# Kernel tuning notes

Measured on AMD Instinct MI355X. Metric: run time of the kernel, lower is better.

The kernel has to match this reference:

```python
import jax, jax.numpy as jnp
import numpy as np

# powers used in the generalized loss (self.range_p); static int constants
RANGE_P = (1, 2)


def setup_inputs() -> dict:
    key = jax.random.key(0)
    k1, k2, k3 = jax.random.split(key, 3)
    n, L, P = 8192, 96, len(RANGE_P)
    y_true = jax.random.normal(k1, (n, L), dtype=jnp.float32)
    y_pred = jax.random.normal(k2, (n, L), dtype=jnp.float32)
    weights = jax.random.uniform(k3, (P, L, L), dtype=jnp.float32)
    return {"y_true": y_true, "y_pred": y_pred, "weights": weights}


def _abs_diff(y_true, y_pred):
    """Vectorized build of the (n, L, L) abs_diff tensor.

    Column j=0:  |y_true - y_pred|  at every position i.
    Column j>=1: rows i in [0, L-j): |(yt[i]-yt[i+j]) - (yp[i]-yp[i+j])|
                 = |e[i] - e[i+j]| with e = y_true - y_pred; zeros elsewhere.
    """
    n, L = y_true.shape
    e = y_true - y_pred                      # (n, L)
    i = jnp.arange(L)[:, None]               # row index (L, 1)
    j = jnp.arange(L)[None, :]               # lag index  (1, L)
    k = i + j                                # partner index (L, L)
    valid = k < L
    kc = jnp.minimum(k, L - 1)               # clipped gather index
    pair = jnp.abs(e[:, :, None] - e[:, kc])  # (n, L, L): |e_i - e_{i+j}|
    D = jnp.where(j == 0,
                  jnp.abs(e)[:, :, None],     # lag-0 column is |e_i|
                  jnp.where(valid, pair, 0.0))
    return D


def reference(y_true, y_pred, weights):
    n, L = y_true.shape
    D = _abs_diff(y_true, y_pred)            # (n, L, L)
    loss = jnp.float32(0.0)
    for p_idx, p in enumerate(RANGE_P):
        # weights[p_idx] is (L, L); broadcasts over the example axis
        loss = loss + jnp.sum(jnp.power(D, p) * weights[p_idx])
    return loss / (L * n)
```

## Files before the change

kernel.cpp:

```cpp
#include <hip/hip_runtime.h>

#define LL 96
#define LPADROW 192
#define NT 256
#define BROWS 16
#define JPT 12
#define NJC 8
#define YBLK 3
#define NSLOT 64

__global__ __launch_bounds__(NT) void gl_loss_main(
    const float* __restrict__ yt, const float* __restrict__ yp,
    const float* __restrict__ w, float* __restrict__ partial, int n) {
  __shared__ float e_lds[BROWS][LPADROW];

  const int t  = threadIdx.x;
  const int c  = blockIdx.y * NT + t;
  const int i  = c >> 3;
  const int jc = c & 7;
  const int j0 = jc * JPT;

  float w0r[JPT], w1r[JPT];
#pragma unroll
  for (int jj = 0; jj < JPT; ++jj) {
    int j = j0 + jj;
    bool valid = (i + j) < LL;
    w0r[jj] = valid ? w[i * LL + j] : 0.f;
    w1r[jj] = valid ? w[LL * LL + i * LL + j] : 0.f;
  }
  const float diagmask = (jc == 0) ? 1.f : 0.f;

  const int b0 = blockIdx.x * BROWS;
  for (int f = t; f < BROWS * LPADROW; f += NT) {
    int row = f / LPADROW;
    int col = f - row * LPADROW;
    float v = 0.f;
    int b = b0 + row;
    if (col < LL && b < n) {
      int g = b * LL + col;
      v = yt[g] - yp[g];
    }
    e_lds[row][col] = v;
  }
  __syncthreads();

  float acc = 0.f;
  for (int b = 0; b < BROWS; ++b) {
    float ei = e_lds[b][i];
    const float* rowp = &e_lds[b][i + j0];
#pragma unroll
    for (int jj = 0; jj < JPT; ++jj) {
      float d = fabsf(ei - rowp[jj]);
      acc = fmaf(d, fmaf(d, w1r[jj], w0r[jj]), acc);
    }
    float a = fabsf(ei) * diagmask;
    acc = fmaf(a, fmaf(a, w1r[0], w0r[0]), acc);
  }

#pragma unroll
  for (int off = 32; off; off >>= 1) acc += __shfl_down(acc, off);
  __shared__ float wsum[NT / 64];
  if ((t & 63) == 0) wsum[t >> 6] = acc;
  __syncthreads();
  if (t == 0) {
    float s = wsum[0] + wsum[1] + wsum[2] + wsum[3];
    atomicAdd(&partial[blockIdx.x & (NSLOT - 1)], s);
  }
}

__global__ __launch_bounds__(64) void gl_loss_fin(
    const float* __restrict__ partial, float* __restrict__ out, float inv_scale) {
  int t = threadIdx.x;
  float v = partial[t];
#pragma unroll
  for (int off = 32; off; off >>= 1) v += __shfl_down(v, off);
  if (t == 0) out[0] = v * inv_scale;
}

extern "C" void kernel_launch(void* const* d_in, const int* in_sizes, int n_in,
                              void* d_out, int out_size, void* d_ws, size_t ws_size,
                              hipStream_t stream) {
  const float* yt = (const float*)d_in[0];
  const float* yp = (const float*)d_in[1];
  const float* w  = (const float*)d_in[2];
  float* out = (float*)d_out;
  int n = in_sizes[0] / LL;

  hipMemsetAsync(d_ws, 0, NSLOT * sizeof(float), stream);

  dim3 grid((n + BROWS - 1) / BROWS, YBLK);
  gl_loss_main<<<grid, NT, 0, stream>>>(yt, yp, w, (float*)d_ws, n);
  gl_loss_fin<<<1, 64, 0, stream>>>((const float*)d_ws, out,
                                    1.0f / (float(LL) * float(n)));
}
```

Baseline: 80.64 us.

## Index pairs by absolute partner column with aligned float4 LDS loads

Each thread now walks absolute partner columns k instead of lags j, so weights are gathered at w[i][k-i] and pairs with k<=i get zero weight. Because every thread in a column group reads the same aligned 12-float slice, it can use three float4 LDS loads. The unaligned per-row pointer reads and the padded 192-wide LDS row go away. Global loads of y_true and y_pred are vectorised to float4, and the accumulation is split into two chains. The lag-0 term now uses separate diagonal weights owned by the thread whose k-range contains i.

```diff
diff --git a/kernel.cpp b/kernel.cpp
--- a/kernel.cpp
+++ b/kernel.cpp
@@ -1,61 +1,72 @@
 #include <hip/hip_runtime.h>
 
 #define LL 96
-#define LPADROW 192
 #define NT 256
 #define BROWS 16
-#define JPT 12
-#define NJC 8
+#define KPT 12
 #define YBLK 3
 #define NSLOT 64
 
 __global__ __launch_bounds__(NT) void gl_loss_main(
     const float* __restrict__ yt, const float* __restrict__ yp,
     const float* __restrict__ w, float* __restrict__ partial, int n) {
-  __shared__ float e_lds[BROWS][LPADROW];
+  __shared__ __align__(16) float e_lds[BROWS][LL];
 
   const int t  = threadIdx.x;
   const int c  = blockIdx.y * NT + t;
   const int i  = c >> 3;
-  const int jc = c & 7;
-  const int j0 = jc * JPT;
+  const int kc = c & 7;
+  const int k0 = kc * KPT;
 
-  float w0r[JPT], w1r[JPT];
+  float w0r[KPT], w1r[KPT];
 #pragma unroll
-  for (int jj = 0; jj < JPT; ++jj) {
-    int j = j0 + jj;
-    bool valid = (i + j) < LL;
-    w0r[jj] = valid ? w[i * LL + j] : 0.f;
-    w1r[jj] = valid ? w[LL * LL + i * LL + j] : 0.f;
+  for (int jj = 0; jj < KPT; ++jj) {
+    int k = k0 + jj;
+    bool valid = (k > i);
+    w0r[jj] = valid ? w[i * LL + (k - i)] : 0.f;
+    w1r[jj] = valid ? w[LL * LL + i * LL + (k - i)] : 0.f;
   }
-  const float diagmask = (jc == 0) ? 1.f : 0.f;
+  const bool dg = (i >= k0) && (i < k0 + KPT);
+  const float w0d = dg ? w[i * LL] : 0.f;
+  const float w1d = dg ? w[LL * LL + i * LL] : 0.f;
 
   const int b0 = blockIdx.x * BROWS;
-  for (int f = t; f < BROWS * LPADROW; f += NT) {
-    int row = f / LPADROW;
-    int col = f - row * LPADROW;
-    float v = 0.f;
+  float4* ef = (float4*)&e_lds[0][0];
+  for (int f = t; f < BROWS * LL / 4; f += NT) {
+    int row = f / (LL / 4);
+    int c4  = f - row * (LL / 4);
     int b = b0 + row;
-    if (col < LL && b < n) {
-      int g = b * LL + col;
-      v = yt[g] - yp[g];
+    float4 v = make_float4(0.f, 0.f, 0.f, 0.f);
+    if (b < n) {
+      const float4 a = *(const float4*)&yt[b * LL + c4 * 4];
+      const float4 p = *(const float4*)&yp[b * LL + c4 * 4];
+      v = make_float4(a.x - p.x, a.y - p.y, a.z - p.z, a.w - p.w);
     }
-    e_lds[row][col] = v;
+    ef[f] = v;
   }
   __syncthreads();
 
-  float acc = 0.f;
+  float acc0 = 0.f, acc1 = 0.f;
+#pragma unroll 2
   for (int b = 0; b < BROWS; ++b) {
     float ei = e_lds[b][i];
-    const float* rowp = &e_lds[b][i + j0];
+    float4 vA = *(const float4*)&e_lds[b][k0];
+    float4 vB = *(const float4*)&e_lds[b][k0 + 4];
+    float4 vC = *(const float4*)&e_lds[b][k0 + 8];
+    float ek[KPT] = {vA.x, vA.y, vA.z, vA.w, vB.x, vB.y, vB.z, vB.w,
+                     vC.x, vC.y, vC.z, vC.w};
 #pragma unroll
-    for (int jj = 0; jj < JPT; ++jj) {
-      float d = fabsf(ei - rowp[jj]);
-      acc = fmaf(d, fmaf(d, w1r[jj], w0r[jj]), acc);
+    for (int jj = 0; jj < KPT; ++jj) {
+      float d = fabsf(ei - ek[jj]);
+      if (jj & 1)
+        acc1 = fmaf(d, fmaf(d, w1r[jj], w0r[jj]), acc1);
+      else
+        acc0 = fmaf(d, fmaf(d, w1r[jj], w0r[jj]), acc0);
     }
-    float a = fabsf(ei) * diagmask;
-    acc = fmaf(a, fmaf(a, w1r[0], w0r[0]), acc);
+    float a = fabsf(ei);
+    acc1 = fmaf(a, fmaf(a, w1d, w0d), acc1);
   }
+  float acc = acc0 + acc1;
 
 #pragma unroll
   for (int off = 32; off; off >>= 1) acc += __shfl_down(acc, off);
```

Result: faster. 76.14 us (-5.6%).
